# Performance work log

Hardware: AMD Instinct MI355X
Metric: run time of the kernel (lower is better)

The kernel has to match this reference:

```python
import jax, jax.numpy as jnp
from jax import lax
import numpy as np

BLOCK = 256
EPS = 1e-6


def rms_norm(x, w):
    var = jnp.mean(jnp.square(x), axis=-1, keepdims=True)
    return x * lax.rsqrt(var + EPS) * w


def lightning_attn(q, k, v, slope):
    # q,k,v: [b,h,n,d]; slope: [h] positive decay rates
    b, h, n, d = q.shape
    nb = n // BLOCK
    ar = jnp.arange(1, BLOCK + 1, dtype=q.dtype)          # [BLOCK]
    s = slope[:, None, None]                               # [h,1,1]
    q_decay = jnp.exp(-s * ar[:, None])                    # [h,BLOCK,1]
    k_decay = jnp.exp(-s * (BLOCK - ar)[:, None])          # [h,BLOCK,1]
    idx = ar[:, None] - ar[None, :]                        # [BLOCK,BLOCK]
    diag_decay = jnp.exp(jnp.where(idx >= 0, -s * idx, -jnp.inf))  # [h,B,B]
    block_decay = jnp.exp(-slope * BLOCK)[None, :, None, None]     # [1,h,1,1]

    def to_blocks(x):
        return jnp.moveaxis(x.reshape(b, h, nb, BLOCK, d), 2, 0)   # [nb,b,h,B,d]

    qb, kb, vb = to_blocks(q), to_blocks(k), to_blocks(v)

    def step(kv, blk):
        qi, ki, vi = blk                                   # [b,h,B,d]
        inter = jnp.einsum('bhmd,bhde->bhme', qi * q_decay, kv)
        qk = jnp.einsum('bhmd,bhkd->bhmk', qi, ki) * diag_decay
        intra = jnp.einsum('bhmk,bhke->bhme', qk, vi)
        kv_new = block_decay * kv + jnp.einsum('bhmd,bhme->bhde', ki * k_decay, vi)
        return kv_new, inter + intra

    kv0 = jnp.zeros((b, h, d, d), q.dtype)
    kv, out = lax.scan(step, kv0, (qb, kb, vb))            # out: [nb,b,h,B,d]
    out = jnp.moveaxis(out, 0, 2).reshape(b, h, n, d)
    return out, kv


def setup_inputs() -> dict:
    key = jax.random.key(0)
    ks = jax.random.split(key, 6)
    b, n, hidden, h, dh = 2, 4096, 2048, 16, 128
    return {
        'hidden_states': jax.random.normal(ks[0], (b, n, hidden), jnp.float32),
        'slope_rate': jax.random.uniform(ks[1], (h,), jnp.float32, 1e-3, 0.2),
        'w_qkv': jax.random.normal(ks[2], (3 * h * dh, hidden), jnp.float32) * 0.02,
        'w_gate': jax.random.normal(ks[3], (h * dh, hidden), jnp.float32) * 0.02,
        'w_out': jax.random.normal(ks[4], (hidden, h * dh), jnp.float32) * 0.02,
        'norm_w': jnp.ones((h * dh,), jnp.float32),
    }


def reference(hidden_states, slope_rate, w_qkv, w_gate, w_out, norm_w):
    b, n, hidden = hidden_states.shape
    h = slope_rate.shape[0]
    dh = hidden // h
    qkv = jax.nn.silu(hidden_states @ w_qkv.T)             # [b,n,3*h*dh]
    qkv = qkv.reshape(b, n, 3, h, dh)
    q = jnp.transpose(qkv[:, :, 0], (0, 2, 1, 3))          # [b,h,n,dh]
    k = jnp.transpose(qkv[:, :, 1], (0, 2, 1, 3))
    v = jnp.transpose(qkv[:, :, 2], (0, 2, 1, 3))
    attn_out, _kv = lightning_attn(q, k, v, slope_rate)
    attn_out = jnp.transpose(attn_out, (0, 2, 1, 3)).reshape(b, n, h * dh)
    out = rms_norm(attn_out, norm_w)
    gate = jax.nn.sigmoid(hidden_states @ w_gate.T)
    out = (gate * out) @ w_out.T
    return out
```

## Files before the change

### kernel.cpp

```cpp
#include <hip/hip_runtime.h>


typedef unsigned short u16;
typedef __bf16 bf16x8 __attribute__((ext_vector_type(8)));
typedef float f32x4 __attribute__((ext_vector_type(4)));

#define SEQ 4096
#define HID 2048

__device__ __forceinline__ u16 f2bf(float f) {
    union { float f; unsigned u; } v; v.f = f;
    unsigned r = v.u + 0x7fffu + ((v.u >> 16) & 1u);
    return (u16)(r >> 16);
}
__device__ __forceinline__ float bf2f(u16 u) {
    union { unsigned u; float f; } v; v.u = ((unsigned)u) << 16; return v.f;
}

typedef __attribute__((address_space(1))) unsigned char gas_u8;
typedef __attribute__((address_space(3))) unsigned char las_u8;
__device__ __forceinline__ void gld16(const void* g, void* l) {
    __builtin_amdgcn_global_load_lds((gas_u8*)g, (las_u8*)l, 16, 0, 0);
}

__global__ __launch_bounds__(256) void castk(const float* __restrict__ in,
                                             u16* __restrict__ out) {
    const size_t i = (size_t)blockIdx.x * 256 + threadIdx.x;
    const float4 f = *(const float4*)&in[i * 4];
    uint2 o;
    o.x = (unsigned)f2bf(f.x) | ((unsigned)f2bf(f.y) << 16);
    o.y = (unsigned)f2bf(f.z) | ((unsigned)f2bf(f.w) << 16);
    *(uint2*)&out[i * 4] = o;
}

template <int MODE>
__global__ __launch_bounds__(512, 2) void gemm256(const u16* __restrict__ A,
                                                  const u16* __restrict__ Bm,
                                                  void* __restrict__ Cv,
                                                  void* __restrict__ aux,
                                                  void* __restrict__ aux2) {
    constexpr int NTN = (MODE == 0) ? 32 : 8;
    constexpr int NT  = 32;
    extern __shared__ u16 smem[];

    const int bid = blockIdx.x;
    const int xcd = bid & 7, l = bid >> 3;
    int tm, tn;
    if constexpr (MODE == 0) {
        tm = xcd * 4 + (l & 3);
        tn = ((l >> 2) & 7) | ((l >> 5) << 3);
    } else {
        const int wgid = xcd * 32 + l;
        tm = wgid / NTN; tn = wgid % NTN;
    }

    const int tid  = threadIdx.x;
    const int lane = tid & 63, wv = tid >> 6;
    const int quad = lane >> 4, cl = lane & 15;
    const int wm = (wv & 1) * 128, wn = (wv >> 1) * 64;

    const int srw  = tid >> 3;
    const int colo = ((tid & 7) ^ (srw & 7)) * 8;
    const u16* gA0 = A  + (size_t)(tm * 256 + srw) * HID + colo;
    const u16* gB0 = Bm + (size_t)(tn * 256 + srw) * HID + colo;

    const int x0 = ((quad       ^ (cl & 7)) * 8);
    const int x1 = (((4 + quad) ^ (cl & 7)) * 8);

    f32x4 acc[8][4];
    const f32x4 zero = {0.f, 0.f, 0.f, 0.f};
    #pragma unroll
    for (int a = 0; a < 8; a++)
        #pragma unroll
        for (int b = 0; b < 4; b++) acc[a][b] = zero;

    bf16x8 af[8], b0[4], b1[4];

    auto STG = [&](int kt, int mat, int hh) {
        const u16* g = (mat ? gB0 : gA0) + (size_t)(hh * 128) * HID + kt * 64;
        u16* lp = smem + (kt & 1) * 32768 + mat * 16384 + hh * 8192 + wv * 512;
        gld16(g, lp);
        gld16(g + (size_t)64 * HID, lp + 4096);
    };
    auto LDA = [&](int qm, int ab) {
        #pragma unroll
        for (int mi = 0; mi < 4; mi++) {
            const int rr = (wm + qm * 64 + mi * 16 + cl) * 64 + ab;
            af[mi * 2 + 0] = *(const bf16x8*)&smem[rr + x0];
            af[mi * 2 + 1] = *(const bf16x8*)&smem[rr + x1];
        }
    };
    auto LDB = [&](bf16x8* d, int qn, int bb2) {
        #pragma unroll
        for (int ni = 0; ni < 2; ni++) {
            const int rr = (wn + qn * 32 + ni * 16 + cl) * 64 + bb2;
            d[ni * 2 + 0] = *(const bf16x8*)&smem[rr + x0];
            d[ni * 2 + 1] = *(const bf16x8*)&smem[rr + x1];
        }
    };
    auto MM = [&](int qm, int qn, const bf16x8* bv) {
        #pragma unroll
        for (int mi = 0; mi < 4; mi++)
            #pragma unroll
            for (int ni = 0; ni < 2; ni++) {
                f32x4 c = acc[qm * 4 + mi][qn * 2 + ni];
                c = __builtin_amdgcn_mfma_f32_16x16x32_bf16(af[mi * 2 + 0], bv[ni * 2 + 0], c, 0, 0, 0);
                c = __builtin_amdgcn_mfma_f32_16x16x32_bf16(af[mi * 2 + 1], bv[ni * 2 + 1], c, 0, 0, 0);
                acc[qm * 4 + mi][qn * 2 + ni] = c;
            }
    };

    STG(0, 1, 0); STG(0, 1, 1); STG(0, 0, 0); STG(0, 0, 1);
    STG(1, 1, 0); STG(1, 1, 1); STG(1, 0, 0);
    asm volatile("s_waitcnt vmcnt(6)" ::: "memory");
    __builtin_amdgcn_s_barrier();
    LDA(0, 0); LDB(b0, 0, 16384);

    #pragma unroll 2
    for (int t = 0; t < NT; ++t) {
        const int ab  = (t & 1) * 32768;
        const int bb2 = ab + 16384;
        const int nab = ((t + 1) & 1) * 32768;
        if (t + 1 < NT) STG(t + 1, 0, 1);
        __builtin_amdgcn_s_barrier();
        asm volatile("s_waitcnt lgkmcnt(0)" ::: "memory");
        __builtin_amdgcn_s_setprio(1); MM(0, 0, b0); __builtin_amdgcn_s_setprio(0);
        LDB(b1, 1, bb2);
        __builtin_amdgcn_s_barrier();
        if (t + 2 < NT) STG(t + 2, 1, 0);
        __builtin_amdgcn_s_barrier();
        asm volatile("s_waitcnt lgkmcnt(0)" ::: "memory");
        __builtin_amdgcn_s_setprio(1); MM(0, 1, b1); __builtin_amdgcn_s_setprio(0);
        LDA(1, ab);
        __builtin_amdgcn_s_barrier();
        if (t + 2 < NT) STG(t + 2, 1, 1);
        __builtin_amdgcn_s_barrier();
        asm volatile("s_waitcnt lgkmcnt(0)" ::: "memory");
        __builtin_amdgcn_s_setprio(1); MM(1, 1, b1); __builtin_amdgcn_s_setprio(0);
        __builtin_amdgcn_s_barrier();
        if (t + 2 < NT) {
            STG(t + 2, 0, 0);
            asm volatile("s_waitcnt vmcnt(6)" ::: "memory");
        } else {
            asm volatile("s_waitcnt vmcnt(0)" ::: "memory");
        }
        __builtin_amdgcn_s_barrier();
        __builtin_amdgcn_s_setprio(1); MM(1, 0, b0); __builtin_amdgcn_s_setprio(0);
        if (t + 1 < NT) { LDA(0, nab); LDB(b0, 0, nab + 16384); }
        __builtin_amdgcn_s_barrier();
    }

    if constexpr (MODE == 0) {
        const int grp = tn * 2 + (wn >> 7);
        const int which = grp >> 4, hd = grp & 15;
        const int n64 = wn & 64;
        if (which == 2) {
            const size_t bz = (size_t)((tm >> 4) * 256 + hd * 16 + (tm & 15));
            u16* tdst = (u16*)aux + bz * 32768;
            #pragma unroll
            for (int a = 0; a < 8; a++) {
                const int mm = wm + (a >> 2) * 64 + (a & 3) * 16 + quad * 4;
                #pragma unroll
                for (int b = 0; b < 4; b++) {
                    const int d = n64 + (b >> 1) * 32 + (b & 1) * 16 + cl;
                    u16 p[4];
                    #pragma unroll
                    for (int r = 0; r < 4; r++) {
                        const float x = acc[a][b][r];
                        p[r] = f2bf(x / (1.f + __expf(-x)));
                    }
                    uint2 pk;
                    pk.x = (unsigned)p[0] | ((unsigned)p[1] << 16);
                    pk.y = (unsigned)p[2] | ((unsigned)p[3] << 16);
                    *(uint2*)&tdst[(size_t)d * 256 + mm] = pk;
                }
            }
            return;
        }
        u16* dst = (which == 0) ? (u16*)Cv
                 : (which == 1) ? (u16*)Cv + (size_t)16777216
                                : (u16*)aux2;
        #pragma unroll
        for (int a = 0; a < 8; a++)
            #pragma unroll
            for (int b = 0; b < 4; b++)
                #pragma unroll
                for (int r = 0; r < 4; r++) {
                    const int m = tm * 256 + wm + (a >> 2) * 64 + (a & 3) * 16 + quad * 4 + r;
                    const int col = hd * 128 + n64 + (b >> 1) * 32 + (b & 1) * 16 + cl;
                    const float x = acc[a][b][r];
                    const float v = (which == 3) ? 1.f / (1.f + __expf(-x))
                                                 : x / (1.f + __expf(-x));
                    dst[(size_t)m * HID + col] = f2bf(v);
                }
        return;
    } else {
        float* C = (float*)Cv;
        #pragma unroll
        for (int a = 0; a < 8; a++)
            #pragma unroll
            for (int b = 0; b < 4; b++)
                #pragma unroll
                for (int r = 0; r < 4; r++) {
                    const int m = tm * 256 + wm + (a >> 2) * 64 + (a & 3) * 16 + quad * 4 + r;
                    const int n = tn * 256 + wn + (b >> 1) * 32 + (b & 1) * 16 + cl;
                    C[(size_t)m * HID + n] = acc[a][b][r];
                }
    }
}

#define M_QKV   0
#define M_P     2
#define M_INTRA 3
#define M_KVT   4
#define M_OUT   6

template <int MODE>
__global__ __launch_bounds__(256) void gemm_nt(const u16* __restrict__ A,
                                               const u16* __restrict__ Bm,
                                               void* __restrict__ Cv,
                                               const float* __restrict__ slope,
                                               int bz0,
                                               void* __restrict__ aux,
                                               void* __restrict__ aux2) {
    constexpr int NPH = (MODE == M_INTRA) ? 2 : 1;
    const int tid = threadIdx.x;
    const int tm = blockIdx.x, tn = blockIdx.y;
    const int bzl = blockIdx.z;
    const int bz  = bzl + bz0;

    int bb = 0, hh = 0, jb = 0;
    if constexpr (MODE == M_P || MODE == M_INTRA || MODE == M_KVT) {
        bb = bz >> 8; hh = (bz >> 4) & 15; jb = bz & 15;
    }

    if constexpr (MODE == M_P) {
        if (tn > tm) {
            u16* C = (u16*)Cv + (size_t)bzl * 65536 + tm * 128 * 256 + tn * 128;
            uint4 z = make_uint4(0u, 0u, 0u, 0u);
            #pragma unroll
            for (int i = 0; i < 8; i++) {
                int f = tid + 256 * i;
                int row = f >> 4, c8 = (f & 15) * 8;
                *(uint4*)&C[row * 256 + c8] = z;
            }
            return;
        }
    }

    __shared__ u16 smem[8192];
    u16 (*As)[32] = (u16(*)[32])smem;
    u16 (*Bs)[32] = (u16(*)[32])(smem + 4096);

    const int lane = tid & 63, wv = tid >> 6;
    const int wm = (wv & 1) * 64, wn = (wv >> 1) * 64;
    const int quad = lane >> 4, cl = lane & 15;
    const int lr = lane >> 2;
    const int lc = (lane & 3) * 8;
    u16* lA = &As[wv * 32][0];
    u16* lB = &Bs[wv * 32][0];

    f32x4 acc[4][4];
    const f32x4 zero = {0.f, 0.f, 0.f, 0.f};
    #pragma unroll
    for (int mi = 0; mi < 4; mi++)
        #pragma unroll
        for (int ni = 0; ni < 4; ni++) acc[mi][ni] = zero;

    #pragma unroll
    for (int ph = 0; ph < NPH; ph++) {
        const u16* Ab; const u16* Bb; int lda, ldb, kmax;
        if constexpr (MODE == M_QKV || MODE == M_OUT) {
            Ab = A; lda = HID; Bb = Bm; ldb = HID; kmax = 2048;
        } else if constexpr (MODE == M_P) {
            const size_t o = ((size_t)(bb * SEQ + jb * 256)) * HID + hh * 128;
            Ab = A + o; lda = HID;
            Bb = Bm + o; ldb = HID;
            kmax = 128;
        } else if constexpr (MODE == M_KVT) {
            Ab = A + (size_t)bz * 32768; lda = 256;
            Bb = Bm + (size_t)bz * 32768; ldb = 256;
            kmax = 256;
        } else {
            if (ph == 0) {
                Ab = A + ((size_t)(bb * SEQ + jb * 256)) * HID + hh * 128; lda = HID;
                Bb = Bm + (size_t)bz * 16384; ldb = 128;
                kmax = 128;
            } else {
                Ab = (const u16*)aux + (size_t)bzl * 65536; lda = 256;
                Bb = (const u16*)aux2 + (size_t)bz * 32768; ldb = 256;
                kmax = (tm == 0) ? 128 : 256;
            }
        }
        const u16* gA = Ab + (size_t)(tm * 128 + wv * 32 + lr) * lda + lc;
        const u16* gB = Bb + (size_t)(tn * 128 + wv * 32 + lr) * ldb + lc;

        for (int k0 = 0; k0 < kmax; k0 += 32) {
            __syncthreads();
            gld16(gA + k0,                    lA);
            gld16(gA + k0 + (size_t)16 * lda, lA + 16 * 32);
            gld16(gB + k0,                    lB);
            gld16(gB + k0 + (size_t)16 * ldb, lB + 16 * 32);
            __syncthreads();
            const int ko = quad * 8;
            bf16x8 af[4], bfv[4];
            #pragma unroll
            for (int mi = 0; mi < 4; mi++) af[mi] = *(const bf16x8*)&As[wm + mi * 16 + cl][ko];
            #pragma unroll
            for (int ni = 0; ni < 4; ni++) bfv[ni] = *(const bf16x8*)&Bs[wn + ni * 16 + cl][ko];
            #pragma unroll
            for (int mi = 0; mi < 4; mi++)
                #pragma unroll
                for (int ni = 0; ni < 4; ni++)
                    acc[mi][ni] = __builtin_amdgcn_mfma_f32_16x16x32_bf16(af[mi], bfv[ni], acc[mi][ni], 0, 0, 0);
        }

        if constexpr (MODE == M_INTRA) {
            if (ph == 0) {
                const float s_ = slope[hh];
                #pragma unroll
                for (int mi = 0; mi < 4; mi++)
                    #pragma unroll
                    for (int r = 0; r < 4; r++) {
                        const int m = tm * 128 + wm + mi * 16 + quad * 4 + r;
                        const float qd = __expf(-s_ * (float)(m + 1));
                        #pragma unroll
                        for (int ni = 0; ni < 4; ni++) acc[mi][ni][r] *= qd;
                    }
            }
        }
    }

    float sl = 0.f;
    if constexpr (MODE == M_P) sl = slope[hh];

    #pragma unroll
    for (int mi = 0; mi < 4; mi++) {
        #pragma unroll
        for (int ni = 0; ni < 4; ni++) {
            const f32x4 v = acc[mi][ni];
            #pragma unroll
            for (int r = 0; r < 4; r++) {
                const int m = tm * 128 + wm + mi * 16 + quad * 4 + r;
                const int n = tn * 128 + wn + ni * 16 + cl;
                const float x = v[r];
                if constexpr (MODE == M_P) {
                    const int d = m - n;
                    ((u16*)Cv)[(size_t)bzl * 65536 + m * 256 + n] =
                        f2bf(d >= 0 ? x * __expf(-sl * (float)d) : 0.f);
                } else if constexpr (MODE == M_INTRA) {
                    ((u16*)Cv)[((size_t)(bb * SEQ + jb * 256 + m)) * HID + hh * 128 + n] = f2bf(x);
                } else if constexpr (MODE == M_KVT) {
                    ((float*)Cv)[(size_t)bz * 16384 + m * 128 + n] = x;
                } else {
                    ((float*)Cv)[(size_t)m * HID + n] = x;
                }
            }
        }
    }
}

__global__ __launch_bounds__(256) void transpose_k(const u16* __restrict__ kb,
                                                   u16* __restrict__ kTs,
                                                   const float* __restrict__ slope) {
    __shared__ u16 t[128][137];
    const int bz = blockIdx.x;
    const int bb = bz >> 8, hh = (bz >> 4) & 15, jb = bz & 15;
    const int tid = threadIdx.x;
    const float s_ = slope[hh];
    const u16* src = kb + ((size_t)(bb * SEQ + jb * 256)) * HID + hh * 128;
    u16* dst = kTs + (size_t)bz * 32768;

    for (int half = 0; half < 2; half++) {
        #pragma unroll
        for (int i = 0; i < 8; i++) {
            const int flat = tid + 256 * i;
            const int row = flat >> 4, c8 = (flat & 15) * 8;
            *(uint4*)&t[row][c8] = *(const uint4*)&src[(size_t)(half * 128 + row) * HID + c8];
        }
        __syncthreads();
        #pragma unroll
        for (int i = 0; i < 8; i++) {
            const int flat = tid + 256 * i;
            const int d = flat >> 4, mc = (flat & 15) * 8;
            u16 p[8];
            #pragma unroll
            for (int j = 0; j < 8; j++) {
                const int m = half * 128 + mc + j;
                p[j] = f2bf(bf2f(t[mc + j][d]) * __expf(-s_ * (float)(255 - m)));
            }
            uint4 pk;
            pk.x = (unsigned)p[0] | ((unsigned)p[1] << 16);
            pk.y = (unsigned)p[2] | ((unsigned)p[3] << 16);
            pk.z = (unsigned)p[4] | ((unsigned)p[5] << 16);
            pk.w = (unsigned)p[6] | ((unsigned)p[7] << 16);
            *(uint4*)&dst[(size_t)d * 256 + half * 128 + mc] = pk;
        }
        __syncthreads();
    }
}

__global__ __launch_bounds__(256) void scan_kv(const float* __restrict__ KVT,
                                               u16* __restrict__ ST,
                                               const float* __restrict__ slope) {
    const int bh = blockIdx.x >> 4, ch = blockIdx.x & 15;
    const int off = ch * 1024 + threadIdx.x * 4;
    const float bd = __expf(-256.f * slope[bh & 15]);
    float4 st = {0.f, 0.f, 0.f, 0.f};
    for (int j = 0; j < 16; j++) {
        const size_t base = ((size_t)(bh * 16 + j)) * 16384 + off;
        uint2 o;
        o.x = (unsigned)f2bf(st.x) | ((unsigned)f2bf(st.y) << 16);
        o.y = (unsigned)f2bf(st.z) | ((unsigned)f2bf(st.w) << 16);
        *(uint2*)&ST[base] = o;
        const float4 kv = *(const float4*)&KVT[base];
        st.x = bd * st.x + kv.x;
        st.y = bd * st.y + kv.y;
        st.z = bd * st.z + kv.z;
        st.w = bd * st.w + kv.w;
    }
}

__global__ __launch_bounds__(256) void rmsnorm_gate(const u16* __restrict__ attn,
                                                    const u16* __restrict__ gate,
                                                    const float* __restrict__ nw,
                                                    u16* __restrict__ y) {
    const int r = blockIdx.x, tid = threadIdx.x;
    const size_t base = (size_t)r * HID + tid * 8;
    const uint4 a = *(const uint4*)&attn[base];
    float x[8];
    x[0] = bf2f(a.x & 0xffff); x[1] = bf2f(a.x >> 16);
    x[2] = bf2f(a.y & 0xffff); x[3] = bf2f(a.y >> 16);
    x[4] = bf2f(a.z & 0xffff); x[5] = bf2f(a.z >> 16);
    x[6] = bf2f(a.w & 0xffff); x[7] = bf2f(a.w >> 16);
    float s = 0.f;
    #pragma unroll
    for (int i = 0; i < 8; i++) s += x[i] * x[i];
    #pragma unroll
    for (int off = 32; off > 0; off >>= 1) s += __shfl_down(s, off);
    __shared__ float red[4];
    if ((tid & 63) == 0) red[tid >> 6] = s;
    __syncthreads();
    const float tot = red[0] + red[1] + red[2] + red[3];
    const float sc = rsqrtf(tot * (1.f / 2048.f) + 1e-6f);
    const uint4 g = *(const uint4*)&gate[base];
    float gv[8];
    gv[0] = bf2f(g.x & 0xffff); gv[1] = bf2f(g.x >> 16);
    gv[2] = bf2f(g.y & 0xffff); gv[3] = bf2f(g.y >> 16);
    gv[4] = bf2f(g.z & 0xffff); gv[5] = bf2f(g.z >> 16);
    gv[6] = bf2f(g.w & 0xffff); gv[7] = bf2f(g.w >> 16);
    const float4 w0 = *(const float4*)&nw[tid * 8];
    const float4 w1 = *(const float4*)&nw[tid * 8 + 4];
    const float wv[8] = {w0.x, w0.y, w0.z, w0.w, w1.x, w1.y, w1.z, w1.w};
    u16 o[8];
    #pragma unroll
    for (int i = 0; i < 8; i++) o[i] = f2bf(gv[i] * x[i] * sc * wv[i]);
    uint4 ov;
    ov.x = (unsigned)o[0] | ((unsigned)o[1] << 16);
    ov.y = (unsigned)o[2] | ((unsigned)o[3] << 16);
    ov.z = (unsigned)o[4] | ((unsigned)o[5] << 16);
    ov.w = (unsigned)o[6] | ((unsigned)o[7] << 16);
    *(uint4*)&y[base] = ov;
}

extern "C" void kernel_launch(void* const* d_in, const int* in_sizes, int n_in,
                              void* d_out, int out_size, void* d_ws, size_t ws_size,
                              hipStream_t stream) {
    const float* hidden = (const float*)d_in[0];
    const float* slope  = (const float*)d_in[1];
    const float* w_qkv  = (const float*)d_in[2];
    const float* w_gate = (const float*)d_in[3];
    const float* w_out  = (const float*)d_in[4];
    const float* norm_w = (const float*)d_in[5];
    float* out = (float*)d_out;

    char* w = (char*)d_ws;
    u16* qb   = (u16*)(w);
    u16* kb   = (u16*)(w +  33554432);
    u16* kTs  = (u16*)(w +  67108864);
    u16* hid_bf = (u16*)(w + 100663296);
    u16* vT   = (u16*)(w + 134217728);
    u16* gate = (u16*)(w + 167772160);
    u16* wqkv_bf  = (u16*)(w + 201326592);
    u16* wgate_bf = (u16*)(w + 201326592 + 25165824);
    float* KVT  = (float*)hid_bf;
    u16*   ST   = kTs;
    u16*   P    = hid_bf;
    u16*   wout_bf = kb;
    u16*   attn = wqkv_bf;
    u16*   y    = kTs;

    static bool s_attr = false;
    if (!s_attr) {
        (void)hipFuncSetAttribute((const void*)gemm256<0>,
                                  hipFuncAttributeMaxDynamicSharedMemorySize, 131072);
        (void)hipFuncSetAttribute((const void*)gemm256<1>,
                                  hipFuncAttributeMaxDynamicSharedMemorySize, 131072);
        s_attr = true;
    }

    castk<<<16384, 256, 0, stream>>>(hidden, hid_bf);
    castk<<<12288, 256, 0, stream>>>(w_qkv,  wqkv_bf);
    castk<<< 4096, 256, 0, stream>>>(w_gate, wgate_bf);

    gemm256<0><<<dim3(1024), dim3(512), 131072, stream>>>(hid_bf, wqkv_bf, qb, vT, gate);
    transpose_k     <<<512,             256, 0, stream>>>(kb, kTs, slope);
    gemm_nt<M_KVT ><<<dim3(1, 1, 512),  256, 0, stream>>>(vT, kTs, KVT, slope, 0, nullptr, nullptr);
    scan_kv         <<<512,             256, 0, stream>>>(KVT, ST, slope);
    gemm_nt<M_P   ><<<dim3(2, 2, 256),  256, 0, stream>>>(qb, kb, P, slope, 0, nullptr, nullptr);
    gemm_nt<M_INTRA><<<dim3(2, 1, 256), 256, 0, stream>>>(qb, ST, attn, slope, 0, P, vT);
    gemm_nt<M_P   ><<<dim3(2, 2, 256),  256, 0, stream>>>(qb, kb, P, slope, 256, nullptr, nullptr);
    gemm_nt<M_INTRA><<<dim3(2, 1, 256), 256, 0, stream>>>(qb, ST, attn, slope, 256, P, vT);
    castk<<< 4096, 256, 0, stream>>>(w_out, wout_bf);
    rmsnorm_gate    <<<8192,            256, 0, stream>>>(attn, gate, norm_w, y);
    gemm256<1><<<dim3(256), dim3(512), 131072, stream>>>(y, wout_bf, (void*)out, nullptr, nullptr);
}
```

Baseline: 476.6 us.

## Fuse intra-block QK^T decay mask and PV into one flash-style kernel

Replaces the separate P-matrix GEMM (which wrote a bf16 decay-masked score matrix to global memory) and the intra/inter output GEMM with a single fused kernel. Each block keeps its Q tile in LDS, first applies the inter-chunk state, then loops over 32-wide K/V slices, computing masked scores into LDS and immediately multiplying by V. This removes the global round-trip of P and two pairs of launches, and processes all 512 block-heads in one launch. In exchange it uses more LDS per block and adds extra barriers per k-step, which may lower occupancy.

```diff
diff --git a/kernel.cpp b/kernel.cpp
--- a/kernel.cpp
+++ b/kernel.cpp
@@ -209,11 +209,7 @@
     }
 }
 
-#define M_QKV   0
-#define M_P     2
-#define M_INTRA 3
 #define M_KVT   4
-#define M_OUT   6
 
 template <int MODE>
 __global__ __launch_bounds__(256) void gemm_nt(const u16* __restrict__ A,
@@ -223,30 +219,8 @@
                                                int bz0,
                                                void* __restrict__ aux,
                                                void* __restrict__ aux2) {
-    constexpr int NPH = (MODE == M_INTRA) ? 2 : 1;
     const int tid = threadIdx.x;
-    const int tm = blockIdx.x, tn = blockIdx.y;
-    const int bzl = blockIdx.z;
-    const int bz  = bzl + bz0;
-
-    int bb = 0, hh = 0, jb = 0;
-    if constexpr (MODE == M_P || MODE == M_INTRA || MODE == M_KVT) {
-        bb = bz >> 8; hh = (bz >> 4) & 15; jb = bz & 15;
-    }
-
-    if constexpr (MODE == M_P) {
-        if (tn > tm) {
-            u16* C = (u16*)Cv + (size_t)bzl * 65536 + tm * 128 * 256 + tn * 128;
-            uint4 z = make_uint4(0u, 0u, 0u, 0u);
-            #pragma unroll
-            for (int i = 0; i < 8; i++) {
-                int f = tid + 256 * i;
-                int row = f >> 4, c8 = (f & 15) * 8;
-                *(uint4*)&C[row * 256 + c8] = z;
-            }
-            return;
-        }
-    }
+    const int bz  = blockIdx.z + bz0;
 
     __shared__ u16 smem[8192];
     u16 (*As)[32] = (u16(*)[32])smem;
@@ -267,97 +241,177 @@
         #pragma unroll
         for (int ni = 0; ni < 4; ni++) acc[mi][ni] = zero;
 
-    #pragma unroll
-    for (int ph = 0; ph < NPH; ph++) {
-        const u16* Ab; const u16* Bb; int lda, ldb, kmax;
-        if constexpr (MODE == M_QKV || MODE == M_OUT) {
-            Ab = A; lda = HID; Bb = Bm; ldb = HID; kmax = 2048;
-        } else if constexpr (MODE == M_P) {
-            const size_t o = ((size_t)(bb * SEQ + jb * 256)) * HID + hh * 128;
-            Ab = A + o; lda = HID;
-            Bb = Bm + o; ldb = HID;
-            kmax = 128;
-        } else if constexpr (MODE == M_KVT) {
-            Ab = A + (size_t)bz * 32768; lda = 256;
-            Bb = Bm + (size_t)bz * 32768; ldb = 256;
-            kmax = 256;
-        } else {
-            if (ph == 0) {
-                Ab = A + ((size_t)(bb * SEQ + jb * 256)) * HID + hh * 128; lda = HID;
-                Bb = Bm + (size_t)bz * 16384; ldb = 128;
-                kmax = 128;
-            } else {
-                Ab = (const u16*)aux + (size_t)bzl * 65536; lda = 256;
-                Bb = (const u16*)aux2 + (size_t)bz * 32768; ldb = 256;
-                kmax = (tm == 0) ? 128 : 256;
-            }
-        }
-        const u16* gA = Ab + (size_t)(tm * 128 + wv * 32 + lr) * lda + lc;
-        const u16* gB = Bb + (size_t)(tn * 128 + wv * 32 + lr) * ldb + lc;
-
-        for (int k0 = 0; k0 < kmax; k0 += 32) {
-            __syncthreads();
-            gld16(gA + k0,                    lA);
-            gld16(gA + k0 + (size_t)16 * lda, lA + 16 * 32);
-            gld16(gB + k0,                    lB);
-            gld16(gB + k0 + (size_t)16 * ldb, lB + 16 * 32);
-            __syncthreads();
-            const int ko = quad * 8;
-            bf16x8 af[4], bfv[4];
-            #pragma unroll
-            for (int mi = 0; mi < 4; mi++) af[mi] = *(const bf16x8*)&As[wm + mi * 16 + cl][ko];
-            #pragma unroll
-            for (int ni = 0; ni < 4; ni++) bfv[ni] = *(const bf16x8*)&Bs[wn + ni * 16 + cl][ko];
-            #pragma unroll
-            for (int mi = 0; mi < 4; mi++)
-                #pragma unroll
-                for (int ni = 0; ni < 4; ni++)
-                    acc[mi][ni] = __builtin_amdgcn_mfma_f32_16x16x32_bf16(af[mi], bfv[ni], acc[mi][ni], 0, 0, 0);
-        }
-
-        if constexpr (MODE == M_INTRA) {
-            if (ph == 0) {
-                const float s_ = slope[hh];
-                #pragma unroll
-                for (int mi = 0; mi < 4; mi++)
-                    #pragma unroll
-                    for (int r = 0; r < 4; r++) {
-                        const int m = tm * 128 + wm + mi * 16 + quad * 4 + r;
-                        const float qd = __expf(-s_ * (float)(m + 1));
-                        #pragma unroll
-                        for (int ni = 0; ni < 4; ni++) acc[mi][ni][r] *= qd;
-                    }
-            }
-        }
-    }
-
-    float sl = 0.f;
-    if constexpr (MODE == M_P) sl = slope[hh];
-
-    #pragma unroll
-    for (int mi = 0; mi < 4; mi++) {
-        #pragma unroll
-        for (int ni = 0; ni < 4; ni++) {
-            const f32x4 v = acc[mi][ni];
+    const u16* Ab = A + (size_t)bz * 32768;
+    const u16* Bb = Bm + (size_t)bz * 32768;
+    const u16* gA = Ab + (size_t)(wv * 32 + lr) * 256 + lc;
+    const u16* gB = Bb + (size_t)(wv * 32 + lr) * 256 + lc;
+
+    for (int k0 = 0; k0 < 256; k0 += 32) {
+        __syncthreads();
+        gld16(gA + k0,                  lA);
+        gld16(gA + k0 + (size_t)16 * 256, lA + 16 * 32);
+        gld16(gB + k0,                  lB);
+        gld16(gB + k0 + (size_t)16 * 256, lB + 16 * 32);
+        __syncthreads();
+        const int ko = quad * 8;
+        bf16x8 af[4], bfv[4];
+        #pragma unroll
+        for (int mi = 0; mi < 4; mi++) af[mi] = *(const bf16x8*)&As[wm + mi * 16 + cl][ko];
+        #pragma unroll
+        for (int ni = 0; ni < 4; ni++) bfv[ni] = *(const bf16x8*)&Bs[wn + ni * 16 + cl][ko];
+        #pragma unroll
+        for (int mi = 0; mi < 4; mi++)
+            #pragma unroll
+            for (int ni = 0; ni < 4; ni++)
+                acc[mi][ni] = __builtin_amdgcn_mfma_f32_16x16x32_bf16(af[mi], bfv[ni], acc[mi][ni], 0, 0, 0);
+    }
+
+    #pragma unroll
+    for (int mi = 0; mi < 4; mi++)
+        #pragma unroll
+        for (int ni = 0; ni < 4; ni++)
+            #pragma unroll
+            for (int r = 0; r < 4; r++) {
+                const int m = wm + mi * 16 + quad * 4 + r;
+                const int n = wn + ni * 16 + cl;
+                ((float*)Cv)[(size_t)bz * 16384 + m * 128 + n] = acc[mi][ni][r];
+            }
+}
+
+__global__ __launch_bounds__(256) void fused_pv(const u16* __restrict__ qb,
+                                                const u16* __restrict__ kb,
+                                                const u16* __restrict__ ST,
+                                                const u16* __restrict__ vT,
+                                                u16* __restrict__ attn,
+                                                const float* __restrict__ slope) {
+    __shared__ u16 smem[28672];
+    u16* q_lds = smem;
+    u16* k_lds = smem + 16384;
+    u16* P_lds = smem + 20480;
+    u16* Bs    = smem + 24576;
+
+    const int tm = blockIdx.x;
+    const int bz = blockIdx.z;
+    const int bb = bz >> 8, hh = (bz >> 4) & 15, jb = bz & 15;
+    const float s_ = slope[hh];
+
+    const int tid  = threadIdx.x;
+    const int lane = tid & 63, wv = tid >> 6;
+    const int quad = lane >> 4, cl = lane & 15;
+    const int wm = (wv & 1) * 64, wn = (wv >> 1) * 64;
+    const int lr = lane >> 2, lc = (lane & 3) * 8;
+    const int pcb = (wv >> 1) * 16;
+
+    const size_t rowbase = (size_t)(bb * SEQ + jb * 256);
+
+    const u16* gq = qb + (rowbase + tm * 128 + wv * 32 + lr) * HID + hh * 128 + lc;
+    u16* lq = q_lds + wv * 1024 + lr * 32 + lc;
+    #pragma unroll
+    for (int ks = 0; ks < 4; ks++) {
+        gld16(gq + ks * 32,                 lq + ks * 4096);
+        gld16(gq + ks * 32 + 16 * HID,      lq + ks * 4096 + 512);
+    }
+
+    f32x4 acc[4][4];
+    const f32x4 zero = {0.f, 0.f, 0.f, 0.f};
+    #pragma unroll
+    for (int mi = 0; mi < 4; mi++)
+        #pragma unroll
+        for (int ni = 0; ni < 4; ni++) acc[mi][ni] = zero;
+
+    const u16* gS = ST + (size_t)bz * 16384 + (size_t)(wv * 32 + lr) * 128 + lc;
+    u16* lB = Bs + wv * 1024 + lr * 32 + lc;
+    #pragma unroll
+    for (int ks = 0; ks < 4; ks++) {
+        __syncthreads();
+        gld16(gS + ks * 32,            lB);
+        gld16(gS + ks * 32 + 16 * 128, lB + 512);
+        __syncthreads();
+        bf16x8 af[4], bfv[4];
+        #pragma unroll
+        for (int mi = 0; mi < 4; mi++)
+            af[mi] = *(const bf16x8*)&q_lds[ks * 4096 + (wm + mi * 16 + cl) * 32 + quad * 8];
+        #pragma unroll
+        for (int ni = 0; ni < 4; ni++)
+            bfv[ni] = *(const bf16x8*)&Bs[(wn + ni * 16 + cl) * 32 + quad * 8];
+        #pragma unroll
+        for (int mi = 0; mi < 4; mi++)
+            #pragma unroll
+            for (int ni = 0; ni < 4; ni++)
+                acc[mi][ni] = __builtin_amdgcn_mfma_f32_16x16x32_bf16(af[mi], bfv[ni], acc[mi][ni], 0, 0, 0);
+    }
+    #pragma unroll
+    for (int mi = 0; mi < 4; mi++)
+        #pragma unroll
+        for (int r = 0; r < 4; r++) {
+            const int m = tm * 128 + wm + mi * 16 + quad * 4 + r;
+            const float qd = __expf(-s_ * (float)(m + 1));
+            #pragma unroll
+            for (int ni = 0; ni < 4; ni++) acc[mi][ni][r] *= qd;
+        }
+
+    const int kmax = (tm == 0) ? 128 : 256;
+    const u16* gV = vT + (size_t)bz * 32768 + (size_t)(wv * 32 + lr) * 256 + lc;
+    const int krow = tid >> 4;
+    const int kcol = (((tid & 15) ^ (krow & 7)) * 8);
+    u16* lk = k_lds + wv * 512 + lane * 8;
+    const int kvr = pcb + cl;
+
+    for (int kv0 = 0; kv0 < kmax; kv0 += 32) {
+        __syncthreads();
+        gld16(kb + (rowbase + kv0 +      krow) * HID + hh * 128 + kcol, lk);
+        gld16(kb + (rowbase + kv0 + 16 + krow) * HID + hh * 128 + kcol, lk + 2048);
+        gld16(gV + kv0,            lB);
+        gld16(gV + kv0 + 16 * 256, lB + 512);
+        __syncthreads();
+        f32x4 acc2[4];
+        #pragma unroll
+        for (int mi = 0; mi < 4; mi++) acc2[mi] = zero;
+        #pragma unroll
+        for (int ds = 0; ds < 4; ds++) {
+            bf16x8 bk = *(const bf16x8*)&k_lds[kvr * 128 + (((ds * 4 + quad) ^ (kvr & 7)) * 8)];
+            #pragma unroll
+            for (int mi = 0; mi < 4; mi++) {
+                bf16x8 aq = *(const bf16x8*)&q_lds[ds * 4096 + (wm + mi * 16 + cl) * 32 + quad * 8];
+                acc2[mi] = __builtin_amdgcn_mfma_f32_16x16x32_bf16(aq, bk, acc2[mi], 0, 0, 0);
+            }
+        }
+        #pragma unroll
+        for (int mi = 0; mi < 4; mi++)
+            #pragma unroll
+            for (int r = 0; r < 4; r++) {
+                const int row = wm + mi * 16 + quad * 4 + r;
+                const int mb  = tm * 128 + row;
+                const int kv  = kv0 + pcb + cl;
+                const int d   = mb - kv;
+                const float x = acc2[mi][r];
+                P_lds[row * 32 + pcb + cl] = f2bf(d >= 0 ? x * __expf(-s_ * (float)d) : 0.f);
+            }
+        __syncthreads();
+        bf16x8 afp[4], bfv[4];
+        #pragma unroll
+        for (int mi = 0; mi < 4; mi++)
+            afp[mi] = *(const bf16x8*)&P_lds[(wm + mi * 16 + cl) * 32 + quad * 8];
+        #pragma unroll
+        for (int ni = 0; ni < 4; ni++)
+            bfv[ni] = *(const bf16x8*)&Bs[(wn + ni * 16 + cl) * 32 + quad * 8];
+        #pragma unroll
+        for (int mi = 0; mi < 4; mi++)
+            #pragma unroll
+            for (int ni = 0; ni < 4; ni++)
+                acc[mi][ni] = __builtin_amdgcn_mfma_f32_16x16x32_bf16(afp[mi], bfv[ni], acc[mi][ni], 0, 0, 0);
+    }
+
+    #pragma unroll
+    for (int mi = 0; mi < 4; mi++)
+        #pragma unroll
+        for (int ni = 0; ni < 4; ni++)
             #pragma unroll
             for (int r = 0; r < 4; r++) {
                 const int m = tm * 128 + wm + mi * 16 + quad * 4 + r;
-                const int n = tn * 128 + wn + ni * 16 + cl;
-                const float x = v[r];
-                if constexpr (MODE == M_P) {
-                    const int d = m - n;
-                    ((u16*)Cv)[(size_t)bzl * 65536 + m * 256 + n] =
-                        f2bf(d >= 0 ? x * __expf(-sl * (float)d) : 0.f);
-                } else if constexpr (MODE == M_INTRA) {
-                    ((u16*)Cv)[((size_t)(bb * SEQ + jb * 256 + m)) * HID + hh * 128 + n] = f2bf(x);
-                } else if constexpr (MODE == M_KVT) {
-                    ((float*)Cv)[(size_t)bz * 16384 + m * 128 + n] = x;
-                } else {
-                    ((float*)Cv)[(size_t)m * HID + n] = x;
-                }
-            }
-        }
-    }
+                const int n = wn + ni * 16 + cl;
+                attn[(rowbase + m) * HID + hh * 128 + n] = f2bf(acc[mi][ni][r]);
+            }
 }
 
 __global__ __launch_bounds__(256) void transpose_k(const u16* __restrict__ kb,
@@ -485,7 +539,6 @@
     u16* wgate_bf = (u16*)(w + 201326592 + 25165824);
     float* KVT  = (float*)hid_bf;
     u16*   ST   = kTs;
-    u16*   P    = hid_bf;
     u16*   wout_bf = kb;
     u16*   attn = wqkv_bf;
     u16*   y    = kTs;
@@ -507,10 +560,7 @@
     transpose_k     <<<512,             256, 0, stream>>>(kb, kTs, slope);
     gemm_nt<M_KVT ><<<dim3(1, 1, 512),  256, 0, stream>>>(vT, kTs, KVT, slope, 0, nullptr, nullptr);
     scan_kv         <<<512,             256, 0, stream>>>(KVT, ST, slope);
-    gemm_nt<M_P   ><<<dim3(2, 2, 256),  256, 0, stream>>>(qb, kb, P, slope, 0, nullptr, nullptr);
-    gemm_nt<M_INTRA><<<dim3(2, 1, 256), 256, 0, stream>>>(qb, ST, attn, slope, 0, P, vT);
-    gemm_nt<M_P   ><<<dim3(2, 2, 256),  256, 0, stream>>>(qb, kb, P, slope, 256, nullptr, nullptr);
-    gemm_nt<M_INTRA><<<dim3(2, 1, 256), 256, 0, stream>>>(qb, ST, attn, slope, 256, P, vT);
+    fused_pv        <<<dim3(2, 1, 512), 256, 0, stream>>>(qb, kb, ST, vT, attn, slope);
     castk<<< 4096, 256, 0, stream>>>(w_out, wout_bf);
     rmsnorm_gate    <<<8192,            256, 0, stream>>>(attn, gate, norm_w, y);
     gemm256<1><<<dim3(256), dim3(512), 131072, stream>>>(y, wout_bf, (void*)out, nullptr, nullptr);
```

New measurement: 447.9 us. -6.0%, faster.
